# Optimization experiments

Measured on AMD Instinct MI355X. Metric: run time of the kernel, lower is better.

## Reference

```python
import jax, jax.numpy as jnp
import numpy as np


def setup_inputs() -> dict:
    key = jax.random.key(0)
    H, W, C, N = 200, 200, 256, 2000
    img = jax.random.normal(key, (1, H, W, C), dtype=jnp.float32)
    rng = np.random.RandomState(0)
    x = rng.randint(0, W - 50, size=N)
    y = rng.randint(0, H - 50, size=N)
    w = rng.randint(8, 50, size=N)
    h = rng.randint(8, 50, size=N)
    rois = jnp.asarray(np.stack([x, y, w, h], axis=-1)[None].astype(np.float32))
    return {"img": img, "rois": rois, "pool_size": 7}


def _roi_bilinear(feat, roi, ps):
    # feat: (H, W, C); roi: int32 (x, y, w, h) -> (ps, ps, C)
    # Mirrors TF1 tf.image.resize_images bilinear, align_corners=False:
    # src coordinate inside the crop = out_idx * (crop_size / ps).
    H, W = feat.shape[0], feat.shape[1]
    x, y, w, h = roi[0], roi[1], roi[2], roi[3]
    sy = h.astype(jnp.float32) / ps
    sx = w.astype(jnp.float32) / ps
    src_y = jnp.arange(ps, dtype=jnp.float32) * sy
    src_x = jnp.arange(ps, dtype=jnp.float32) * sx
    y0 = jnp.floor(src_y).astype(jnp.int32)
    x0 = jnp.floor(src_x).astype(jnp.int32)
    wy = src_y - y0.astype(jnp.float32)
    wx = src_x - x0.astype(jnp.float32)
    # clamp inside the crop, then translate to global image coords (and clamp for safety)
    gy0 = jnp.clip(y + jnp.clip(y0, 0, h - 1), 0, H - 1)
    gy1 = jnp.clip(y + jnp.clip(y0 + 1, 0, h - 1), 0, H - 1)
    gx0 = jnp.clip(x + jnp.clip(x0, 0, w - 1), 0, W - 1)
    gx1 = jnp.clip(x + jnp.clip(x0 + 1, 0, w - 1), 0, W - 1)
    v00 = feat[gy0[:, None], gx0[None, :]]  # (ps, ps, C)
    v01 = feat[gy0[:, None], gx1[None, :]]
    v10 = feat[gy1[:, None], gx0[None, :]]
    v11 = feat[gy1[:, None], gx1[None, :]]
    wy = wy[:, None, None]
    wx = wx[None, :, None]
    top = v00 * (1.0 - wx) + v01 * wx
    bot = v10 * (1.0 - wx) + v11 * wx
    return top * (1.0 - wy) + bot * wy


def reference(img, rois, pool_size):
    feat = img[0]                          # (H, W, C)
    roi_int = rois[0].astype(jnp.int32)    # (N, 4) -- cast as in the 'tf' branch
    pooled = jax.vmap(lambda r: _roi_bilinear(feat, r, pool_size))(roi_int)
    return pooled[None]                    # (1, N, ps, ps, C)
```

## Files before the change

kernel.cpp:

```cpp
#include <hip/hip_runtime.h>
#include <hip/hip_bf16.h>


__global__ __launch_bounds__(256) void RoIPool_53575422050620_kernel(
    const float* __restrict__ feat,
    const float* __restrict__ rois,
    const int*   __restrict__ psp,
    float*       __restrict__ out,
    int n_cells, int H, int W, int C)
{
    const int ps   = psp[0];
    const int cell = blockIdx.x * 4 + (threadIdx.x >> 6);
    if (cell >= n_cells) return;
    const int lane = threadIdx.x & 63;

    const int pp  = ps * ps;
    const int roi = cell / pp;
    const int rem = cell - roi * pp;
    const int py  = rem / ps;
    const int px  = rem - py * ps;

    const float4 r = reinterpret_cast<const float4*>(rois)[roi];
    const int x = (int)r.x;
    const int y = (int)r.y;
    const int w = (int)r.z;
    const int h = (int)r.w;

    const float sy    = (float)h / (float)ps;
    const float sx    = (float)w / (float)ps;
    const float src_y = (float)py * sy;
    const float src_x = (float)px * sx;
    const int y0 = (int)floorf(src_y);
    const int x0 = (int)floorf(src_x);
    const float wy = src_y - (float)y0;
    const float wx = src_x - (float)x0;

    const int gy0 = min(max(y + min(max(y0,     0), h - 1), 0), H - 1);
    const int gy1 = min(max(y + min(max(y0 + 1, 0), h - 1), 0), H - 1);
    const int gx0 = min(max(x + min(max(x0,     0), w - 1), 0), W - 1);
    const int gx1 = min(max(x + min(max(x0 + 1, 0), w - 1), 0), W - 1);

    const int C4 = C >> 2;
    const float4* __restrict__ f4 = reinterpret_cast<const float4*>(feat);
    float4* __restrict__ o4 = reinterpret_cast<float4*>(out);

    const size_t b00 = (size_t)(gy0 * W + gx0) * C4;
    const size_t b01 = (size_t)(gy0 * W + gx1) * C4;
    const size_t b10 = (size_t)(gy1 * W + gx0) * C4;
    const size_t b11 = (size_t)(gy1 * W + gx1) * C4;
    const size_t ob  = (size_t)cell * C4;

    const float omwx = 1.0f - wx;
    const float omwy = 1.0f - wy;

    for (int cv = lane; cv < C4; cv += 64) {
        const float4 v00 = f4[b00 + cv];
        const float4 v01 = f4[b01 + cv];
        const float4 v10 = f4[b10 + cv];
        const float4 v11 = f4[b11 + cv];
        float4 o;
        o.x = (v00.x * omwx + v01.x * wx) * omwy + (v10.x * omwx + v11.x * wx) * wy;
        o.y = (v00.y * omwx + v01.y * wx) * omwy + (v10.y * omwx + v11.y * wx) * wy;
        o.z = (v00.z * omwx + v01.z * wx) * omwy + (v10.z * omwx + v11.z * wx) * wy;
        o.w = (v00.w * omwx + v01.w * wx) * omwy + (v10.w * omwx + v11.w * wx) * wy;
        o4[ob + cv] = o;
    }
}

extern "C" void kernel_launch(void* const* d_in, const int* in_sizes, int n_in,
                              void* d_out, int out_size, void* d_ws, size_t ws_size,
                              hipStream_t stream) {
    const float* img  = (const float*)d_in[0];
    const float* rois = (const float*)d_in[1];
    const int*   psp  = (const int*)d_in[2];
    float*       out  = (float*)d_out;

    const int H = 200, W = 200, C = 256;
    const int n_cells = out_size / C;
    const int blocks  = (n_cells + 3) / 4;

    RoIPool_53575422050620_kernel<<<blocks, 256, 0, stream>>>(
        img, rois, psp, out, n_cells, H, W, C);
}
```

Before: 166.9 us.

## Process a full pooled row per wavefront with unrolled bilinear gathers

Each wavefront now computes all ps cells of one output row instead of a single cell, sharing the row/ROI setup and issuing unrolled independent gathers for the 7 columns. Output stores use nontemporal hints and vector-extension arithmetic. The host grid assumes pool size 7 and the kernel assumes C equals 256 (one float4 per lane), reducing generality.

```diff
diff --git a/kernel.cpp b/kernel.cpp
--- a/kernel.cpp
+++ b/kernel.cpp
@@ -1,24 +1,23 @@
 #include <hip/hip_runtime.h>
 #include <hip/hip_bf16.h>
 
+
+typedef float f32x4 __attribute__((ext_vector_type(4)));
 
 __global__ __launch_bounds__(256) void RoIPool_53575422050620_kernel(
     const float* __restrict__ feat,
     const float* __restrict__ rois,
     const int*   __restrict__ psp,
     float*       __restrict__ out,
-    int n_cells, int H, int W, int C)
+    int n_rows, int H, int W, int C)
 {
-    const int ps   = psp[0];
-    const int cell = blockIdx.x * 4 + (threadIdx.x >> 6);
-    if (cell >= n_cells) return;
+    const int ps  = psp[0];
+    const int row = blockIdx.x * 4 + (threadIdx.x >> 6);
+    if (row >= n_rows) return;
     const int lane = threadIdx.x & 63;
 
-    const int pp  = ps * ps;
-    const int roi = cell / pp;
-    const int rem = cell - roi * pp;
-    const int py  = rem / ps;
-    const int px  = rem - py * ps;
+    const int roi = row / ps;
+    const int py  = row - roi * ps;
 
     const float4 r = reinterpret_cast<const float4*>(rois)[roi];
     const int x = (int)r.x;
@@ -29,41 +28,47 @@
     const float sy    = (float)h / (float)ps;
     const float sx    = (float)w / (float)ps;
     const float src_y = (float)py * sy;
-    const float src_x = (float)px * sx;
-    const int y0 = (int)floorf(src_y);
-    const int x0 = (int)floorf(src_x);
-    const float wy = src_y - (float)y0;
-    const float wx = src_x - (float)x0;
+    const int   y0    = (int)floorf(src_y);
+    const float wy    = src_y - (float)y0;
+    const float omwy  = 1.0f - wy;
 
     const int gy0 = min(max(y + min(max(y0,     0), h - 1), 0), H - 1);
     const int gy1 = min(max(y + min(max(y0 + 1, 0), h - 1), 0), H - 1);
-    const int gx0 = min(max(x + min(max(x0,     0), w - 1), 0), W - 1);
-    const int gx1 = min(max(x + min(max(x0 + 1, 0), w - 1), 0), W - 1);
 
     const int C4 = C >> 2;
-    const float4* __restrict__ f4 = reinterpret_cast<const float4*>(feat);
-    float4* __restrict__ o4 = reinterpret_cast<float4*>(out);
+    const f32x4* __restrict__ f4 = reinterpret_cast<const f32x4*>(feat);
+    f32x4* __restrict__ o4 = reinterpret_cast<f32x4*>(out);
 
-    const size_t b00 = (size_t)(gy0 * W + gx0) * C4;
-    const size_t b01 = (size_t)(gy0 * W + gx1) * C4;
-    const size_t b10 = (size_t)(gy1 * W + gx0) * C4;
-    const size_t b11 = (size_t)(gy1 * W + gx1) * C4;
-    const size_t ob  = (size_t)cell * C4;
+    const size_t r0 = (size_t)(gy0 * W) * C4 + lane;
+    const size_t r1 = (size_t)(gy1 * W) * C4 + lane;
+    const size_t ob = (size_t)row * ps * C4 + lane;
 
-    const float omwx = 1.0f - wx;
-    const float omwy = 1.0f - wy;
+    auto body = [&](int px) {
+        const float src_x = (float)px * sx;
+        const int   x0    = (int)floorf(src_x);
+        const float wx    = src_x - (float)x0;
+        const float omwx  = 1.0f - wx;
 
-    for (int cv = lane; cv < C4; cv += 64) {
-        const float4 v00 = f4[b00 + cv];
-        const float4 v01 = f4[b01 + cv];
-        const float4 v10 = f4[b10 + cv];
-        const float4 v11 = f4[b11 + cv];
-        float4 o;
-        o.x = (v00.x * omwx + v01.x * wx) * omwy + (v10.x * omwx + v11.x * wx) * wy;
-        o.y = (v00.y * omwx + v01.y * wx) * omwy + (v10.y * omwx + v11.y * wx) * wy;
-        o.z = (v00.z * omwx + v01.z * wx) * omwy + (v10.z * omwx + v11.z * wx) * wy;
-        o.w = (v00.w * omwx + v01.w * wx) * omwy + (v10.w * omwx + v11.w * wx) * wy;
-        o4[ob + cv] = o;
+        const int gx0 = min(max(x + min(max(x0,     0), w - 1), 0), W - 1);
+        const int gx1 = min(max(x + min(max(x0 + 1, 0), w - 1), 0), W - 1);
+
+        const f32x4 v00 = f4[r0 + (size_t)gx0 * C4];
+        const f32x4 v01 = f4[r0 + (size_t)gx1 * C4];
+        const f32x4 v10 = f4[r1 + (size_t)gx0 * C4];
+        const f32x4 v11 = f4[r1 + (size_t)gx1 * C4];
+
+        const f32x4 top = v00 * omwx + v01 * wx;
+        const f32x4 bot = v10 * omwx + v11 * wx;
+        const f32x4 o   = top * omwy + bot * wy;
+
+        __builtin_nontemporal_store(o, &o4[ob + (size_t)px * C4]);
+    };
+
+    if (ps == 7) {
+#pragma unroll
+        for (int px = 0; px < 7; ++px) body(px);
+    } else {
+        for (int px = 0; px < ps; ++px) body(px);
     }
 }
 
@@ -76,9 +81,10 @@
     float*       out  = (float*)d_out;
 
     const int H = 200, W = 200, C = 256;
-    const int n_cells = out_size / C;
-    const int blocks  = (n_cells + 3) / 4;
+    const int ps = 7;
+    const int n_rows = out_size / (C * ps);
+    const int blocks = (n_rows + 3) / 4;
 
     RoIPool_53575422050620_kernel<<<blocks, 256, 0, stream>>>(
-        img, rois, psp, out, n_cells, H, W, C);
+        img, rois, psp, out, n_rows, H, W, C);
 }
```

Measured after the change: 169.3 us. No clear change (+1.5%).
